# Kernel tuning notes

Hardware: AMD Instinct MI355X
Metric: run time of the kernel (lower is better)

The kernel has to match this reference:

```python
import jax, jax.numpy as jnp
import numpy as np

B, H, W = 4, 1024, 1024
V, F, T = 98304, 196608, 131072
EPS = 1e-8


def setup_inputs() -> dict:
    key = jax.random.key(0)
    k = jax.random.split(key, 6)
    # screen-space vertices: xy in pixel coords, z (depth) in [0.5, 5.5)
    xy = jax.random.uniform(k[0], (B, V, 2), dtype=jnp.float32) * jnp.array([W, H], jnp.float32)
    z = jax.random.uniform(k[1], (B, V, 1), dtype=jnp.float32) * 5.0 + 0.5
    v2d = jnp.concatenate([xy, z], axis=-1)
    vt = jax.random.uniform(k[2], (T, 2), dtype=jnp.float32)
    vi = jax.random.randint(k[3], (F, 3), 0, V, dtype=jnp.int32)
    vti = jax.random.randint(k[4], (F, 3), 0, T, dtype=jnp.int32)
    # -1 marks background pixels (mask), as in the original renderer
    index_img = jax.random.randint(k[5], (B, H, W), -1, F, dtype=jnp.int32)
    vn = jax.random.normal(jax.random.fold_in(key, 7), (B, V, 3), dtype=jnp.float32)
    return {"v2d": v2d, "vt": vt, "vi": vi, "vti": vti, "index_img": index_img, "vn": vn}


def _epsclamp(x):
    return jnp.where(x < 0, jnp.minimum(x, -EPS), jnp.maximum(x, EPS))


def _gather_b(table, idx):
    # table [B,N,C], idx [B,H,W] -> [B,H,W,C]
    return jax.vmap(lambda t, i: t[i])(table, idx)


def reference(v2d, vt, vi, vti, index_img, vn):
    h, w = index_img.shape[1], index_img.shape[2]
    pcy, pcx = jnp.meshgrid(jnp.arange(h, dtype=v2d.dtype), jnp.arange(w, dtype=v2d.dtype), indexing="ij")
    mask = index_img != -1                       # [B,H,W]
    fm = mask.astype(v2d.dtype)                  # [B,H,W]
    ii = jnp.maximum(index_img, 0)               # [B,H,W]

    vi_img = vi[ii]                              # [B,H,W,3] vertex ids per pixel
    p0 = _gather_b(v2d, vi_img[..., 0])          # [B,H,W,3]
    p1 = _gather_b(v2d, vi_img[..., 1])
    p2 = _gather_b(v2d, vi_img[..., 2])

    vec01 = p1 - p0
    vec02 = p2 - p0
    det = vec01[..., 0] * vec02[..., 1] - vec01[..., 1] * vec02[..., 0]
    denom = _epsclamp(det)
    px = pcx[None] - p0[..., 0]
    py = pcy[None] - p0[..., 1]
    l1 = (px * vec02[..., 1] - py * vec02[..., 0]) / denom
    l2 = (py * vec01[..., 0] - px * vec01[..., 1]) / denom
    l0 = 1.0 - l1 - l2

    w0 = 1.0 / _epsclamp(p0[..., 2])
    w1 = 1.0 / _epsclamp(p1[..., 2])
    w2 = 1.0 / _epsclamp(p2[..., 2])
    zi = 1.0 / _epsclamp(w0 * l0 + w1 * l1 + w2 * l2)
    b0 = w0 * l0 * zi
    b1 = w1 * l1 * zi
    b2 = w2 * l2 * zi
    bary_img = jnp.stack([b0, b1, b2], axis=-1) * fm[..., None]   # [B,H,W,3]

    vti_img = vti[ii]                            # [B,H,W,3]
    t0 = vt[vti_img[..., 0]]                     # [B,H,W,2] (shared uv table)
    t1 = vt[vti_img[..., 1]]
    t2 = vt[vti_img[..., 2]]
    vt_img = t0 * b0[..., None] + t1 * b1[..., None] + t2 * b2[..., None]

    depth_img = zi * fm

    base = jnp.stack([(pcx * 2 + 1) / w, (pcy * 2 + 1) / h], axis=-1) - 1.0  # [H,W,2]
    vt_img = base[None] + fm[..., None] * ((vt_img * 2 - 1) - base[None])    # lerp

    n0 = _gather_b(vn, vi_img[..., 0])
    n1 = _gather_b(vn, vi_img[..., 1])
    n2 = _gather_b(vn, vi_img[..., 2])
    vn_img = (n0 * bary_img[..., 0:1] + n1 * bary_img[..., 1:2] + n2 * bary_img[..., 2:3]) * fm[..., None]

    return depth_img, bary_img, vt_img, vn_img
```

## Files before the change

kernel.cpp:

```cpp
#include <hip/hip_runtime.h>


#define EPSV 1e-8f

__device__ __forceinline__ float epsclamp(float x) {
    return x < 0.0f ? fminf(x, -EPSV) : fmaxf(x, EPSV);
}

constexpr int Wd = 1024, Hd = 1024, Vd = 98304;
constexpr int NPIX = 4 * 1024 * 1024;
constexpr int PIX_PER_BATCH = 1024 * 1024;

struct I3 { int a, b, c; };
struct F3 { float x, y, z; };

__device__ __forceinline__ int swizzled_pixel(int j, int tid) {
    const int xcd = j & 7;
    const int b = xcd >> 1;
    const int sub = ((j >> 3) << 1) + (j & 1);
    return b * PIX_PER_BATCH + sub * 256 + tid;
}

__global__ __launch_bounds__(256) void passA(
    const float* __restrict__ v2d,
    const int*   __restrict__ vi,
    const int*   __restrict__ index_img,
    const float* __restrict__ vn,
    float* __restrict__ out)
{
#pragma clang fp contract(off)
    const int p = swizzled_pixel(blockIdx.x, threadIdx.x);

    const int x = p & (Wd - 1);
    const int y = (p >> 10) & (Hd - 1);
    const int b = p >> 20;

    const int idx = index_img[p];
    const float fm = (idx != -1) ? 1.0f : 0.0f;
    const int f = (idx < 0) ? 0 : idx;

    const I3 ii = *reinterpret_cast<const I3*>(vi + 3 * (size_t)f);

    const float* __restrict__ vb = v2d + (size_t)b * Vd * 3;
    const F3 P0 = *reinterpret_cast<const F3*>(vb + 3 * (size_t)ii.a);
    const F3 P1 = *reinterpret_cast<const F3*>(vb + 3 * (size_t)ii.b);
    const F3 P2 = *reinterpret_cast<const F3*>(vb + 3 * (size_t)ii.c);

    const float* __restrict__ nb = vn + (size_t)b * Vd * 3;
    const F3 N0 = *reinterpret_cast<const F3*>(nb + 3 * (size_t)ii.a);
    const F3 N1 = *reinterpret_cast<const F3*>(nb + 3 * (size_t)ii.b);
    const F3 N2 = *reinterpret_cast<const F3*>(nb + 3 * (size_t)ii.c);

    const float v01x = P1.x - P0.x, v01y = P1.y - P0.y;
    const float v02x = P2.x - P0.x, v02y = P2.y - P0.y;
    const float det = (v01x * v02y) - (v01y * v02x);
    const float denom = epsclamp(det);
    const float pxr = (float)x - P0.x;
    const float pyr = (float)y - P0.y;
    const float l1 = ((pxr * v02y) - (pyr * v02x)) / denom;
    const float l2 = ((pyr * v01x) - (pxr * v01y)) / denom;
    const float l0 = (1.0f - l1) - l2;

    const float w0 = 1.0f / epsclamp(P0.z);
    const float w1 = 1.0f / epsclamp(P1.z);
    const float w2 = 1.0f / epsclamp(P2.z);
    const float t0w = w0 * l0;
    const float t1w = w1 * l1;
    const float t2w = w2 * l2;
    const float zsum = (t0w + t1w) + t2w;
    const float zi = 1.0f / epsclamp(zsum);

    const float b0m = (t0w * zi) * fm;
    const float b1m = (t1w * zi) * fm;
    const float b2m = (t2w * zi) * fm;

    const float vnx = (((N0.x * b0m) + (N1.x * b1m)) + (N2.x * b2m)) * fm;
    const float vny = (((N0.y * b0m) + (N1.y * b1m)) + (N2.y * b2m)) * fm;
    const float vnz = (((N0.z * b0m) + (N1.z * b1m)) + (N2.z * b2m)) * fm;

    out[p] = zi * fm;
    float* __restrict__ out_bary = out + (size_t)NPIX;
    out_bary[3 * (size_t)p + 0] = b0m;
    out_bary[3 * (size_t)p + 1] = b1m;
    out_bary[3 * (size_t)p + 2] = b2m;
    float* __restrict__ out_vn = out + (size_t)NPIX * 6;
    out_vn[3 * (size_t)p + 0] = vnx;
    out_vn[3 * (size_t)p + 1] = vny;
    out_vn[3 * (size_t)p + 2] = vnz;
}

__global__ __launch_bounds__(256) void passB(
    const float* __restrict__ vt,
    const int*   __restrict__ vti,
    const int*   __restrict__ index_img,
    float* __restrict__ out)
{
#pragma clang fp contract(off)
    const int p = blockIdx.x * 256 + threadIdx.x;

    const int x = p & (Wd - 1);
    const int y = (p >> 10) & (Hd - 1);

    const int idx = index_img[p];
    const float fm = (idx != -1) ? 1.0f : 0.0f;
    const int f = (idx < 0) ? 0 : idx;

    const I3 tt = *reinterpret_cast<const I3*>(vti + 3 * (size_t)f);

    const float* __restrict__ bary = out + (size_t)NPIX;
    const float b0 = bary[3 * (size_t)p + 0];
    const float b1 = bary[3 * (size_t)p + 1];
    const float b2 = bary[3 * (size_t)p + 2];

    const float2* __restrict__ vt2 = reinterpret_cast<const float2*>(vt);
    const float2 tA = vt2[tt.a];
    const float2 tB = vt2[tt.b];
    const float2 tC = vt2[tt.c];
    float vtx = ((tA.x * b0) + (tB.x * b1)) + (tC.x * b2);
    float vty = ((tA.y * b0) + (tB.y * b1)) + (tC.y * b2);

    const float bx = (((float)x * 2.0f) + 1.0f) / (float)Wd - 1.0f;
    const float by = (((float)y * 2.0f) + 1.0f) / (float)Hd - 1.0f;
    vtx = bx + (fm * (((vtx * 2.0f) - 1.0f) - bx));
    vty = by + (fm * (((vty * 2.0f) - 1.0f) - by));

    float* __restrict__ out_vt = out + (size_t)NPIX * 4;
    reinterpret_cast<float2*>(out_vt)[p] = make_float2(vtx, vty);
}

extern "C" void kernel_launch(void* const* d_in, const int* in_sizes, int n_in,
                              void* d_out, int out_size, void* d_ws, size_t ws_size,
                              hipStream_t stream) {
    const float* v2d       = (const float*)d_in[0];
    const float* vt        = (const float*)d_in[1];
    const int*   vi        = (const int*)d_in[2];
    const int*   vti       = (const int*)d_in[3];
    const int*   index_img = (const int*)d_in[4];
    const float* vn        = (const float*)d_in[5];
    float* out = (float*)d_out;

    dim3 grid(NPIX / 256), block(256);
    passA<<<grid, block, 0, stream>>>(v2d, vi, index_img, vn, out);
    passB<<<grid, block, 0, stream>>>(vt, vti, index_img, out);
}
```

Baseline: 219.2 us.

## Split normals into third pass and process four pixels per thread with vector I/O

Pass A is split so positions and normals are gathered in separate kernels, each with a smaller random-access working set (v2d per batch, then vn per batch), plus a third launch. Every thread now handles four consecutive pixels, using int4 index loads and float4 stores or reloads of depth, barycentrics, UVs and normals instead of scalar strided stores. The cost is an extra launch, a re-read of index_img, vi and the barycentric buffer, and more registers per thread, which can lower occupancy for latency-bound gathers.

```diff
diff --git a/kernel.cpp b/kernel.cpp
--- a/kernel.cpp
+++ b/kernel.cpp
@@ -8,85 +8,138 @@
 }
 
 constexpr int Wd = 1024, Hd = 1024, Vd = 98304;
-constexpr int NPIX = 4 * 1024 * 1024;
-constexpr int PIX_PER_BATCH = 1024 * 1024;
+constexpr int NPIX = 1 << 22;
+constexpr int PPB  = 1 << 20;
 
 struct I3 { int a, b, c; };
 struct F3 { float x, y, z; };
 
-__device__ __forceinline__ int swizzled_pixel(int j, int tid) {
+__device__ __forceinline__ int base_pixel_swz(int j, int tid) {
     const int xcd = j & 7;
     const int b = xcd >> 1;
     const int sub = ((j >> 3) << 1) + (j & 1);
-    return b * PIX_PER_BATCH + sub * 256 + tid;
-}
-
-__global__ __launch_bounds__(256) void passA(
+    return b * PPB + sub * 1024 + tid * 4;
+}
+
+__global__ __launch_bounds__(256) void pass1(
     const float* __restrict__ v2d,
     const int*   __restrict__ vi,
     const int*   __restrict__ index_img,
-    const float* __restrict__ vn,
     float* __restrict__ out)
 {
 #pragma clang fp contract(off)
-    const int p = swizzled_pixel(blockIdx.x, threadIdx.x);
-
-    const int x = p & (Wd - 1);
-    const int y = (p >> 10) & (Hd - 1);
-    const int b = p >> 20;
-
-    const int idx = index_img[p];
-    const float fm = (idx != -1) ? 1.0f : 0.0f;
-    const int f = (idx < 0) ? 0 : idx;
-
-    const I3 ii = *reinterpret_cast<const I3*>(vi + 3 * (size_t)f);
+    const int pb = base_pixel_swz(blockIdx.x, threadIdx.x);
+    const int b = pb >> 20;
+
+    const int4 iv = *reinterpret_cast<const int4*>(index_img + pb);
+    const int idx[4] = { iv.x, iv.y, iv.z, iv.w };
+
+    I3 ii[4];
+#pragma unroll
+    for (int k = 0; k < 4; ++k) {
+        const int f = idx[k] < 0 ? 0 : idx[k];
+        ii[k] = *reinterpret_cast<const I3*>(vi + 3 * (size_t)f);
+    }
 
     const float* __restrict__ vb = v2d + (size_t)b * Vd * 3;
-    const F3 P0 = *reinterpret_cast<const F3*>(vb + 3 * (size_t)ii.a);
-    const F3 P1 = *reinterpret_cast<const F3*>(vb + 3 * (size_t)ii.b);
-    const F3 P2 = *reinterpret_cast<const F3*>(vb + 3 * (size_t)ii.c);
+    F3 P0[4], P1[4], P2[4];
+#pragma unroll
+    for (int k = 0; k < 4; ++k) {
+        P0[k] = *reinterpret_cast<const F3*>(vb + 3 * (size_t)ii[k].a);
+        P1[k] = *reinterpret_cast<const F3*>(vb + 3 * (size_t)ii[k].b);
+        P2[k] = *reinterpret_cast<const F3*>(vb + 3 * (size_t)ii[k].c);
+    }
+
+    float dep[4], b0m[4], b1m[4], b2m[4];
+#pragma unroll
+    for (int k = 0; k < 4; ++k) {
+        const int p = pb + k;
+        const int x = p & (Wd - 1);
+        const int y = (p >> 10) & (Hd - 1);
+        const float fm = (idx[k] != -1) ? 1.0f : 0.0f;
+
+        const float v01x = P1[k].x - P0[k].x, v01y = P1[k].y - P0[k].y;
+        const float v02x = P2[k].x - P0[k].x, v02y = P2[k].y - P0[k].y;
+        const float det = (v01x * v02y) - (v01y * v02x);
+        const float denom = epsclamp(det);
+        const float pxr = (float)x - P0[k].x;
+        const float pyr = (float)y - P0[k].y;
+        const float l1 = ((pxr * v02y) - (pyr * v02x)) / denom;
+        const float l2 = ((pyr * v01x) - (pxr * v01y)) / denom;
+        const float l0 = (1.0f - l1) - l2;
+
+        const float w0 = 1.0f / epsclamp(P0[k].z);
+        const float w1 = 1.0f / epsclamp(P1[k].z);
+        const float w2 = 1.0f / epsclamp(P2[k].z);
+        const float t0w = w0 * l0;
+        const float t1w = w1 * l1;
+        const float t2w = w2 * l2;
+        const float zsum = (t0w + t1w) + t2w;
+        const float zi = 1.0f / epsclamp(zsum);
+
+        dep[k] = zi * fm;
+        b0m[k] = (t0w * zi) * fm;
+        b1m[k] = (t1w * zi) * fm;
+        b2m[k] = (t2w * zi) * fm;
+    }
+
+    *reinterpret_cast<float4*>(out + pb) = make_float4(dep[0], dep[1], dep[2], dep[3]);
+    float* __restrict__ ob = out + (size_t)NPIX + 3 * (size_t)pb;
+    reinterpret_cast<float4*>(ob)[0] = make_float4(b0m[0], b1m[0], b2m[0], b0m[1]);
+    reinterpret_cast<float4*>(ob)[1] = make_float4(b1m[1], b2m[1], b0m[2], b1m[2]);
+    reinterpret_cast<float4*>(ob)[2] = make_float4(b2m[2], b0m[3], b1m[3], b2m[3]);
+}
+
+__global__ __launch_bounds__(256) void pass3(
+    const float* __restrict__ vn,
+    const int*   __restrict__ vi,
+    const int*   __restrict__ index_img,
+    float* __restrict__ out)
+{
+#pragma clang fp contract(off)
+    const int pb = base_pixel_swz(blockIdx.x, threadIdx.x);
+    const int b = pb >> 20;
+
+    const int4 iv = *reinterpret_cast<const int4*>(index_img + pb);
+    const int idx[4] = { iv.x, iv.y, iv.z, iv.w };
+
+    I3 ii[4];
+#pragma unroll
+    for (int k = 0; k < 4; ++k) {
+        const int f = idx[k] < 0 ? 0 : idx[k];
+        ii[k] = *reinterpret_cast<const I3*>(vi + 3 * (size_t)f);
+    }
 
     const float* __restrict__ nb = vn + (size_t)b * Vd * 3;
-    const F3 N0 = *reinterpret_cast<const F3*>(nb + 3 * (size_t)ii.a);
-    const F3 N1 = *reinterpret_cast<const F3*>(nb + 3 * (size_t)ii.b);
-    const F3 N2 = *reinterpret_cast<const F3*>(nb + 3 * (size_t)ii.c);
-
-    const float v01x = P1.x - P0.x, v01y = P1.y - P0.y;
-    const float v02x = P2.x - P0.x, v02y = P2.y - P0.y;
-    const float det = (v01x * v02y) - (v01y * v02x);
-    const float denom = epsclamp(det);
-    const float pxr = (float)x - P0.x;
-    const float pyr = (float)y - P0.y;
-    const float l1 = ((pxr * v02y) - (pyr * v02x)) / denom;
-    const float l2 = ((pyr * v01x) - (pxr * v01y)) / denom;
-    const float l0 = (1.0f - l1) - l2;
-
-    const float w0 = 1.0f / epsclamp(P0.z);
-    const float w1 = 1.0f / epsclamp(P1.z);
-    const float w2 = 1.0f / epsclamp(P2.z);
-    const float t0w = w0 * l0;
-    const float t1w = w1 * l1;
-    const float t2w = w2 * l2;
-    const float zsum = (t0w + t1w) + t2w;
-    const float zi = 1.0f / epsclamp(zsum);
-
-    const float b0m = (t0w * zi) * fm;
-    const float b1m = (t1w * zi) * fm;
-    const float b2m = (t2w * zi) * fm;
-
-    const float vnx = (((N0.x * b0m) + (N1.x * b1m)) + (N2.x * b2m)) * fm;
-    const float vny = (((N0.y * b0m) + (N1.y * b1m)) + (N2.y * b2m)) * fm;
-    const float vnz = (((N0.z * b0m) + (N1.z * b1m)) + (N2.z * b2m)) * fm;
-
-    out[p] = zi * fm;
-    float* __restrict__ out_bary = out + (size_t)NPIX;
-    out_bary[3 * (size_t)p + 0] = b0m;
-    out_bary[3 * (size_t)p + 1] = b1m;
-    out_bary[3 * (size_t)p + 2] = b2m;
-    float* __restrict__ out_vn = out + (size_t)NPIX * 6;
-    out_vn[3 * (size_t)p + 0] = vnx;
-    out_vn[3 * (size_t)p + 1] = vny;
-    out_vn[3 * (size_t)p + 2] = vnz;
+    F3 N0[4], N1[4], N2[4];
+#pragma unroll
+    for (int k = 0; k < 4; ++k) {
+        N0[k] = *reinterpret_cast<const F3*>(nb + 3 * (size_t)ii[k].a);
+        N1[k] = *reinterpret_cast<const F3*>(nb + 3 * (size_t)ii[k].b);
+        N2[k] = *reinterpret_cast<const F3*>(nb + 3 * (size_t)ii[k].c);
+    }
+
+    const float* __restrict__ bp = out + (size_t)NPIX + 3 * (size_t)pb;
+    const float4 B0 = reinterpret_cast<const float4*>(bp)[0];
+    const float4 B1 = reinterpret_cast<const float4*>(bp)[1];
+    const float4 B2 = reinterpret_cast<const float4*>(bp)[2];
+    const float b0m[4] = { B0.x, B0.w, B1.z, B2.y };
+    const float b1m[4] = { B0.y, B1.x, B1.w, B2.z };
+    const float b2m[4] = { B0.z, B1.y, B2.x, B2.w };
+
+    float vnx[4], vny[4], vnz[4];
+#pragma unroll
+    for (int k = 0; k < 4; ++k) {
+        const float fm = (idx[k] != -1) ? 1.0f : 0.0f;
+        vnx[k] = (((N0[k].x * b0m[k]) + (N1[k].x * b1m[k])) + (N2[k].x * b2m[k])) * fm;
+        vny[k] = (((N0[k].y * b0m[k]) + (N1[k].y * b1m[k])) + (N2[k].y * b2m[k])) * fm;
+        vnz[k] = (((N0[k].z * b0m[k]) + (N1[k].z * b1m[k])) + (N2[k].z * b2m[k])) * fm;
+    }
+
+    float* __restrict__ on = out + (size_t)NPIX * 6 + 3 * (size_t)pb;
+    reinterpret_cast<float4*>(on)[0] = make_float4(vnx[0], vny[0], vnz[0], vnx[1]);
+    reinterpret_cast<float4*>(on)[1] = make_float4(vny[1], vnz[1], vnx[2], vny[2]);
+    reinterpret_cast<float4*>(on)[2] = make_float4(vnz[2], vnx[3], vny[3], vnz[3]);
 }
 
 __global__ __launch_bounds__(256) void passB(
@@ -96,36 +149,55 @@
     float* __restrict__ out)
 {
 #pragma clang fp contract(off)
-    const int p = blockIdx.x * 256 + threadIdx.x;
-
-    const int x = p & (Wd - 1);
-    const int y = (p >> 10) & (Hd - 1);
-
-    const int idx = index_img[p];
-    const float fm = (idx != -1) ? 1.0f : 0.0f;
-    const int f = (idx < 0) ? 0 : idx;
-
-    const I3 tt = *reinterpret_cast<const I3*>(vti + 3 * (size_t)f);
-
-    const float* __restrict__ bary = out + (size_t)NPIX;
-    const float b0 = bary[3 * (size_t)p + 0];
-    const float b1 = bary[3 * (size_t)p + 1];
-    const float b2 = bary[3 * (size_t)p + 2];
+    const int pb = blockIdx.x * 1024 + threadIdx.x * 4;
+
+    const int4 iv = *reinterpret_cast<const int4*>(index_img + pb);
+    const int idx[4] = { iv.x, iv.y, iv.z, iv.w };
+
+    I3 tt[4];
+#pragma unroll
+    for (int k = 0; k < 4; ++k) {
+        const int f = idx[k] < 0 ? 0 : idx[k];
+        tt[k] = *reinterpret_cast<const I3*>(vti + 3 * (size_t)f);
+    }
 
     const float2* __restrict__ vt2 = reinterpret_cast<const float2*>(vt);
-    const float2 tA = vt2[tt.a];
-    const float2 tB = vt2[tt.b];
-    const float2 tC = vt2[tt.c];
-    float vtx = ((tA.x * b0) + (tB.x * b1)) + (tC.x * b2);
-    float vty = ((tA.y * b0) + (tB.y * b1)) + (tC.y * b2);
-
-    const float bx = (((float)x * 2.0f) + 1.0f) / (float)Wd - 1.0f;
-    const float by = (((float)y * 2.0f) + 1.0f) / (float)Hd - 1.0f;
-    vtx = bx + (fm * (((vtx * 2.0f) - 1.0f) - bx));
-    vty = by + (fm * (((vty * 2.0f) - 1.0f) - by));
-
-    float* __restrict__ out_vt = out + (size_t)NPIX * 4;
-    reinterpret_cast<float2*>(out_vt)[p] = make_float2(vtx, vty);
+    float2 tA[4], tB[4], tC[4];
+#pragma unroll
+    for (int k = 0; k < 4; ++k) {
+        tA[k] = vt2[tt[k].a];
+        tB[k] = vt2[tt[k].b];
+        tC[k] = vt2[tt[k].c];
+    }
+
+    const float* __restrict__ bp = out + (size_t)NPIX + 3 * (size_t)pb;
+    const float4 B0 = reinterpret_cast<const float4*>(bp)[0];
+    const float4 B1 = reinterpret_cast<const float4*>(bp)[1];
+    const float4 B2 = reinterpret_cast<const float4*>(bp)[2];
+    const float b0[4] = { B0.x, B0.w, B1.z, B2.y };
+    const float b1[4] = { B0.y, B1.x, B1.w, B2.z };
+    const float b2[4] = { B0.z, B1.y, B2.x, B2.w };
+
+    float u[4], v[4];
+#pragma unroll
+    for (int k = 0; k < 4; ++k) {
+        const int p = pb + k;
+        const int x = p & (Wd - 1);
+        const int y = (p >> 10) & (Hd - 1);
+        const float fm = (idx[k] != -1) ? 1.0f : 0.0f;
+
+        float vtx = ((tA[k].x * b0[k]) + (tB[k].x * b1[k])) + (tC[k].x * b2[k]);
+        float vty = ((tA[k].y * b0[k]) + (tB[k].y * b1[k])) + (tC[k].y * b2[k]);
+
+        const float bx = (((float)x * 2.0f) + 1.0f) / (float)Wd - 1.0f;
+        const float by = (((float)y * 2.0f) + 1.0f) / (float)Hd - 1.0f;
+        u[k] = bx + (fm * (((vtx * 2.0f) - 1.0f) - bx));
+        v[k] = by + (fm * (((vty * 2.0f) - 1.0f) - by));
+    }
+
+    float* __restrict__ ov = out + (size_t)NPIX * 4 + 2 * (size_t)pb;
+    reinterpret_cast<float4*>(ov)[0] = make_float4(u[0], v[0], u[1], v[1]);
+    reinterpret_cast<float4*>(ov)[1] = make_float4(u[2], v[2], u[3], v[3]);
 }
 
 extern "C" void kernel_launch(void* const* d_in, const int* in_sizes, int n_in,
@@ -139,7 +211,8 @@
     const float* vn        = (const float*)d_in[5];
     float* out = (float*)d_out;
 
-    dim3 grid(NPIX / 256), block(256);
-    passA<<<grid, block, 0, stream>>>(v2d, vi, index_img, vn, out);
+    dim3 grid(NPIX / 1024), block(256);
+    pass1<<<grid, block, 0, stream>>>(v2d, vi, index_img, out);
     passB<<<grid, block, 0, stream>>>(vt, vti, index_img, out);
-}
+    pass3<<<grid, block, 0, stream>>>(vn, vi, index_img, out);
+}
```

Result: slower. 249.1 us (+13.7%).

## Repack vertex tables to float4 and vectorize UV pass over four pixels per thread

Applied to the files above, without the earlier changes.

Adds a pre-pass that copies the per-batch vertex position and normal tables into 16-byte padded float4 arrays in workspace, so the main pass gathers each vertex with one aligned load instead of three scalar loads. The UV pass now handles four consecutive pixels per thread, using int4 loads for indices, float4 loads for barycentrics and float4 stores for UVs. The repack adds an extra launch plus about 12 MB of workspace traffic, and the original path is kept as a fallback when workspace is too small.

```diff
diff --git a/kernel.cpp b/kernel.cpp
--- a/kernel.cpp
+++ b/kernel.cpp
@@ -7,9 +7,15 @@
     return x < 0.0f ? fminf(x, -EPSV) : fmaxf(x, EPSV);
 }
 
-constexpr int Wd = 1024, Hd = 1024, Vd = 98304;
-constexpr int NPIX = 4 * 1024 * 1024;
-constexpr int PIX_PER_BATCH = 1024 * 1024;
+constexpr int Wd = 1024, Hd = 1024, Vd = 98304, Fd = 196608, Bd = 4;
+constexpr int NPIX = 1 << 22;
+constexpr int PPB  = 1 << 20;
+
+constexpr size_t OFF_V2DP = 0;
+constexpr size_t SZ_V2DP  = (size_t)Bd * Vd * 16;
+constexpr size_t OFF_VNP  = OFF_V2DP + SZ_V2DP;
+constexpr size_t SZ_VNP   = (size_t)Bd * Vd * 16;
+constexpr size_t WS_NEED  = OFF_VNP + SZ_VNP;
 
 struct I3 { int a, b, c; };
 struct F3 { float x, y, z; };
@@ -18,19 +24,25 @@
     const int xcd = j & 7;
     const int b = xcd >> 1;
     const int sub = ((j >> 3) << 1) + (j & 1);
-    return b * PIX_PER_BATCH + sub * 256 + tid;
-}
-
-__global__ __launch_bounds__(256) void passA(
-    const float* __restrict__ v2d,
-    const int*   __restrict__ vi,
-    const int*   __restrict__ index_img,
-    const float* __restrict__ vn,
-    float* __restrict__ out)
+    return b * PPB + sub * 256 + tid;
+}
+
+__global__ __launch_bounds__(256) void repack_vert(
+    const float* __restrict__ v2d, const float* __restrict__ vn,
+    float4* __restrict__ v2dp, float4* __restrict__ vnp)
+{
+    const int i = blockIdx.x * 256 + threadIdx.x;
+    v2dp[i] = make_float4(v2d[3 * (size_t)i], v2d[3 * (size_t)i + 1], v2d[3 * (size_t)i + 2], 0.f);
+    vnp[i]  = make_float4(vn[3 * (size_t)i],  vn[3 * (size_t)i + 1],  vn[3 * (size_t)i + 2],  0.f);
+}
+
+__global__ __launch_bounds__(256) void passAx(
+    const float4* __restrict__ v2dp, const float4* __restrict__ vnp,
+    const int* __restrict__ vi,
+    const int* __restrict__ index_img, float* __restrict__ out)
 {
 #pragma clang fp contract(off)
     const int p = swizzled_pixel(blockIdx.x, threadIdx.x);
-
     const int x = p & (Wd - 1);
     const int y = (p >> 10) & (Hd - 1);
     const int b = p >> 20;
@@ -39,17 +51,18 @@
     const float fm = (idx != -1) ? 1.0f : 0.0f;
     const int f = (idx < 0) ? 0 : idx;
 
-    const I3 ii = *reinterpret_cast<const I3*>(vi + 3 * (size_t)f);
-
-    const float* __restrict__ vb = v2d + (size_t)b * Vd * 3;
-    const F3 P0 = *reinterpret_cast<const F3*>(vb + 3 * (size_t)ii.a);
-    const F3 P1 = *reinterpret_cast<const F3*>(vb + 3 * (size_t)ii.b);
-    const F3 P2 = *reinterpret_cast<const F3*>(vb + 3 * (size_t)ii.c);
-
-    const float* __restrict__ nb = vn + (size_t)b * Vd * 3;
-    const F3 N0 = *reinterpret_cast<const F3*>(nb + 3 * (size_t)ii.a);
-    const F3 N1 = *reinterpret_cast<const F3*>(nb + 3 * (size_t)ii.b);
-    const F3 N2 = *reinterpret_cast<const F3*>(nb + 3 * (size_t)ii.c);
+    const int i0 = vi[3 * (size_t)f + 0];
+    const int i1 = vi[3 * (size_t)f + 1];
+    const int i2 = vi[3 * (size_t)f + 2];
+
+    const float4* __restrict__ vb = v2dp + (size_t)b * Vd;
+    const float4* __restrict__ nb = vnp + (size_t)b * Vd;
+    const float4 P0 = vb[i0];
+    const float4 P1 = vb[i1];
+    const float4 P2 = vb[i2];
+    const float4 N0 = nb[i0];
+    const float4 N1 = nb[i1];
+    const float4 N2 = nb[i2];
 
     const float v01x = P1.x - P0.x, v01y = P1.y - P0.y;
     const float v02x = P2.x - P0.x, v02y = P2.y - P0.y;
@@ -79,53 +92,120 @@
     const float vnz = (((N0.z * b0m) + (N1.z * b1m)) + (N2.z * b2m)) * fm;
 
     out[p] = zi * fm;
-    float* __restrict__ out_bary = out + (size_t)NPIX;
-    out_bary[3 * (size_t)p + 0] = b0m;
-    out_bary[3 * (size_t)p + 1] = b1m;
-    out_bary[3 * (size_t)p + 2] = b2m;
-    float* __restrict__ out_vn = out + (size_t)NPIX * 6;
-    out_vn[3 * (size_t)p + 0] = vnx;
-    out_vn[3 * (size_t)p + 1] = vny;
-    out_vn[3 * (size_t)p + 2] = vnz;
-}
-
-__global__ __launch_bounds__(256) void passB(
-    const float* __restrict__ vt,
-    const int*   __restrict__ vti,
-    const int*   __restrict__ index_img,
+    float* __restrict__ ob = out + (size_t)NPIX;
+    ob[3 * (size_t)p + 0] = b0m;
+    ob[3 * (size_t)p + 1] = b1m;
+    ob[3 * (size_t)p + 2] = b2m;
+    float* __restrict__ on = out + (size_t)NPIX * 6;
+    on[3 * (size_t)p + 0] = vnx;
+    on[3 * (size_t)p + 1] = vny;
+    on[3 * (size_t)p + 2] = vnz;
+}
+
+__global__ __launch_bounds__(256) void passAf(
+    const float* __restrict__ v2d, const int* __restrict__ vi,
+    const int* __restrict__ index_img, const float* __restrict__ vn,
     float* __restrict__ out)
 {
 #pragma clang fp contract(off)
-    const int p = blockIdx.x * 256 + threadIdx.x;
-
+    const int p = swizzled_pixel(blockIdx.x, threadIdx.x);
     const int x = p & (Wd - 1);
     const int y = (p >> 10) & (Hd - 1);
+    const int b = p >> 20;
 
     const int idx = index_img[p];
     const float fm = (idx != -1) ? 1.0f : 0.0f;
     const int f = (idx < 0) ? 0 : idx;
 
-    const I3 tt = *reinterpret_cast<const I3*>(vti + 3 * (size_t)f);
-
-    const float* __restrict__ bary = out + (size_t)NPIX;
-    const float b0 = bary[3 * (size_t)p + 0];
-    const float b1 = bary[3 * (size_t)p + 1];
-    const float b2 = bary[3 * (size_t)p + 2];
-
+    const I3 ii = *reinterpret_cast<const I3*>(vi + 3 * (size_t)f);
+    const float* __restrict__ vb = v2d + (size_t)b * Vd * 3;
+    const F3 P0 = *reinterpret_cast<const F3*>(vb + 3 * (size_t)ii.a);
+    const F3 P1 = *reinterpret_cast<const F3*>(vb + 3 * (size_t)ii.b);
+    const F3 P2 = *reinterpret_cast<const F3*>(vb + 3 * (size_t)ii.c);
+    const float* __restrict__ nb = vn + (size_t)b * Vd * 3;
+    const F3 N0 = *reinterpret_cast<const F3*>(nb + 3 * (size_t)ii.a);
+    const F3 N1 = *reinterpret_cast<const F3*>(nb + 3 * (size_t)ii.b);
+    const F3 N2 = *reinterpret_cast<const F3*>(nb + 3 * (size_t)ii.c);
+
+    const float v01x = P1.x - P0.x, v01y = P1.y - P0.y;
+    const float v02x = P2.x - P0.x, v02y = P2.y - P0.y;
+    const float det = (v01x * v02y) - (v01y * v02x);
+    const float denom = epsclamp(det);
+    const float pxr = (float)x - P0.x;
+    const float pyr = (float)y - P0.y;
+    const float l1 = ((pxr * v02y) - (pyr * v02x)) / denom;
+    const float l2 = ((pyr * v01x) - (pxr * v01y)) / denom;
+    const float l0 = (1.0f - l1) - l2;
+    const float w0 = 1.0f / epsclamp(P0.z);
+    const float w1 = 1.0f / epsclamp(P1.z);
+    const float w2 = 1.0f / epsclamp(P2.z);
+    const float t0w = w0 * l0, t1w = w1 * l1, t2w = w2 * l2;
+    const float zsum = (t0w + t1w) + t2w;
+    const float zi = 1.0f / epsclamp(zsum);
+    const float b0m = (t0w * zi) * fm;
+    const float b1m = (t1w * zi) * fm;
+    const float b2m = (t2w * zi) * fm;
+    const float vnx = (((N0.x * b0m) + (N1.x * b1m)) + (N2.x * b2m)) * fm;
+    const float vny = (((N0.y * b0m) + (N1.y * b1m)) + (N2.y * b2m)) * fm;
+    const float vnz = (((N0.z * b0m) + (N1.z * b1m)) + (N2.z * b2m)) * fm;
+
+    out[p] = zi * fm;
+    float* __restrict__ ob = out + (size_t)NPIX;
+    ob[3 * (size_t)p + 0] = b0m;
+    ob[3 * (size_t)p + 1] = b1m;
+    ob[3 * (size_t)p + 2] = b2m;
+    float* __restrict__ on = out + (size_t)NPIX * 6;
+    on[3 * (size_t)p + 0] = vnx;
+    on[3 * (size_t)p + 1] = vny;
+    on[3 * (size_t)p + 2] = vnz;
+}
+
+__global__ __launch_bounds__(256) void passBf(
+    const float* __restrict__ vt, const int* __restrict__ vti,
+    const int* __restrict__ index_img, float* __restrict__ out)
+{
+#pragma clang fp contract(off)
+    const int pb = blockIdx.x * 1024 + threadIdx.x * 4;
+    const int4 iv = *reinterpret_cast<const int4*>(index_img + pb);
+    const int idx[4] = { iv.x, iv.y, iv.z, iv.w };
+    I3 tt[4];
+#pragma unroll
+    for (int k = 0; k < 4; ++k) {
+        const int f = idx[k] < 0 ? 0 : idx[k];
+        tt[k] = *reinterpret_cast<const I3*>(vti + 3 * (size_t)f);
+    }
     const float2* __restrict__ vt2 = reinterpret_cast<const float2*>(vt);
-    const float2 tA = vt2[tt.a];
-    const float2 tB = vt2[tt.b];
-    const float2 tC = vt2[tt.c];
-    float vtx = ((tA.x * b0) + (tB.x * b1)) + (tC.x * b2);
-    float vty = ((tA.y * b0) + (tB.y * b1)) + (tC.y * b2);
-
-    const float bx = (((float)x * 2.0f) + 1.0f) / (float)Wd - 1.0f;
-    const float by = (((float)y * 2.0f) + 1.0f) / (float)Hd - 1.0f;
-    vtx = bx + (fm * (((vtx * 2.0f) - 1.0f) - bx));
-    vty = by + (fm * (((vty * 2.0f) - 1.0f) - by));
-
-    float* __restrict__ out_vt = out + (size_t)NPIX * 4;
-    reinterpret_cast<float2*>(out_vt)[p] = make_float2(vtx, vty);
+    float2 tA[4], tB[4], tC[4];
+#pragma unroll
+    for (int k = 0; k < 4; ++k) {
+        tA[k] = vt2[tt[k].a];
+        tB[k] = vt2[tt[k].b];
+        tC[k] = vt2[tt[k].c];
+    }
+    const float* __restrict__ bp = out + (size_t)NPIX + 3 * (size_t)pb;
+    const float4 B0 = reinterpret_cast<const float4*>(bp)[0];
+    const float4 B1 = reinterpret_cast<const float4*>(bp)[1];
+    const float4 B2 = reinterpret_cast<const float4*>(bp)[2];
+    const float b0[4] = { B0.x, B0.w, B1.z, B2.y };
+    const float b1[4] = { B0.y, B1.x, B1.w, B2.z };
+    const float b2[4] = { B0.z, B1.y, B2.x, B2.w };
+    float u[4], v[4];
+#pragma unroll
+    for (int k = 0; k < 4; ++k) {
+        const int p = pb + k;
+        const int x = p & (Wd - 1);
+        const int y = (p >> 10) & (Hd - 1);
+        const float fm = (idx[k] != -1) ? 1.0f : 0.0f;
+        float vtx = ((tA[k].x * b0[k]) + (tB[k].x * b1[k])) + (tC[k].x * b2[k]);
+        float vty = ((tA[k].y * b0[k]) + (tB[k].y * b1[k])) + (tC[k].y * b2[k]);
+        const float bx = (((float)x * 2.0f) + 1.0f) / (float)Wd - 1.0f;
+        const float by = (((float)y * 2.0f) + 1.0f) / (float)Hd - 1.0f;
+        u[k] = bx + (fm * (((vtx * 2.0f) - 1.0f) - bx));
+        v[k] = by + (fm * (((vty * 2.0f) - 1.0f) - by));
+    }
+    float* __restrict__ ov = out + (size_t)NPIX * 4 + 2 * (size_t)pb;
+    reinterpret_cast<float4*>(ov)[0] = make_float4(u[0], v[0], u[1], v[1]);
+    reinterpret_cast<float4*>(ov)[1] = make_float4(u[2], v[2], u[3], v[3]);
 }
 
 extern "C" void kernel_launch(void* const* d_in, const int* in_sizes, int n_in,
@@ -139,7 +219,16 @@
     const float* vn        = (const float*)d_in[5];
     float* out = (float*)d_out;
 
-    dim3 grid(NPIX / 256), block(256);
-    passA<<<grid, block, 0, stream>>>(v2d, vi, index_img, vn, out);
-    passB<<<grid, block, 0, stream>>>(vt, vti, index_img, out);
-}
+    dim3 block(256);
+
+    if (ws_size >= WS_NEED) {
+        char* ws = (char*)d_ws;
+        float4* v2dp = (float4*)(ws + OFF_V2DP);
+        float4* vnp  = (float4*)(ws + OFF_VNP);
+        repack_vert<<<dim3(Bd * Vd / 256), block, 0, stream>>>(v2d, vn, v2dp, vnp);
+        passAx<<<dim3(NPIX / 256), block, 0, stream>>>(v2dp, vnp, vi, index_img, out);
+    } else {
+        passAf<<<dim3(NPIX / 256), block, 0, stream>>>(v2d, vi, index_img, vn, out);
+    }
+    passBf<<<dim3(NPIX / 1024), block, 0, stream>>>(vt, vti, index_img, out);
+}
```

After: 241.5 us. 10.2% more time.
